# Kernel optimization log

Measured on AMD Instinct MI355X. Metric: run time of the kernel, lower is better.

## Reference

```python
import jax, jax.numpy as jnp
import numpy as np

S_DIM = 128            # attention head width s
E_DIM = 1024           # expansion e = 2*hidden
SQRT_S = 128.0 ** 0.5
EPS = 1e-5


def setup_inputs() -> dict:
    key = jax.random.key(0)
    ks = jax.random.split(key, 8)
    B, S, H = 64, 512, 512
    uv_dim = 2 * E_DIM + S_DIM  # 2176
    # xavier-uniform-ish scale for uv weight
    lim = (6.0 / (H + uv_dim)) ** 0.5
    return {
        "x": jax.random.normal(ks[0], (B, S, H), dtype=jnp.float32),
        "ln_g": jnp.ones((1,), dtype=jnp.float32),
        "uv_w": jax.random.uniform(ks[1], (uv_dim, H), minval=-lim, maxval=lim, dtype=jnp.float32),
        "uv_b": jnp.zeros((uv_dim,), dtype=jnp.float32),
        "gamma": jax.random.uniform(ks[2], (2, S_DIM), dtype=jnp.float32),
        "beta": jax.random.uniform(ks[3], (2, S_DIM), dtype=jnp.float32),
        "w_bias": jax.random.uniform(ks[4], (2 * S - 1,), dtype=jnp.float32),
        "o_w": jax.random.normal(ks[5], (H, E_DIM), dtype=jnp.float32) * 0.02,
        "o_b": jnp.zeros((H,), dtype=jnp.float32),
    }


def _rope(x):
    # x: [B, S, 2, s]; rotate along the sequence dim (dim=1)
    S = x.shape[1]
    half = x.shape[-1] // 2
    pos = jnp.arange(S, dtype=jnp.float32)
    # torch: freq_seq = -arange(half)/half; inv_freq = 10000**(-freq_seq)
    inv_freq = 10000.0 ** (jnp.arange(half, dtype=jnp.float32) / half)
    sinus = pos[:, None, None] * inv_freq[None, None, :]  # [S, 1, half]
    sin, cos = jnp.sin(sinus), jnp.cos(sinus)
    x1, x2 = x[..., :half], x[..., half:]
    return jnp.concatenate([x1 * cos - x2 * sin, x2 * cos + x1 * sin], axis=-1)


def reference(x, ln_g, uv_w, uv_b, gamma, beta, w_bias, o_w, o_b):
    B, S, H = x.shape
    # ScaleNorm
    norm = jnp.linalg.norm(x, axis=-1, keepdims=True) * (H ** -0.5)
    xn = x / jnp.maximum(norm, EPS) * ln_g
    # fused uv projection + SiLU
    act = jax.nn.silu(xn @ uv_w.T + uv_b)  # [B, S, 2e+s]
    u = act[..., :E_DIM]
    v = act[..., E_DIM:2 * E_DIM]
    base = act[..., 2 * E_DIM:]                      # [B, S, s]
    base = base[:, :, None, :] * gamma + beta        # [B, S, 2, s]
    base = _rope(base)
    q, k = base[:, :, 0, :], base[:, :, 1, :]
    # scores + relative position bias: bias[i, j] = w[j - i + S - 1]
    qk = jnp.einsum('bsd,btd->bst', q, k)
    idx = jnp.arange(S)[None, :] - jnp.arange(S)[:, None] + (S - 1)
    qk = qk + w_bias[idx]
    # relu2 similarity kernel
    kernel = jnp.square(jax.nn.relu(qk / SQRT_S))    # [B, S, S]
    out = u * jnp.einsum('bst,bte->bse', kernel, v)  # gated attention
    out = out @ o_w.T + o_b
    return out + x  # use_shortcut: hidden == output
```

## Files before the change

kernel.cpp:

```cpp
#include <hip/hip_runtime.h>
#include <math.h>


#define M_TOT   32768
#define S_LEN   512
#define H_DIM   512
#define E_DIMC  1024
#define UV_DIM  2176
#define UV_PAD  2304
#define D_DIM   128

using floatx4  = __attribute__((ext_vector_type(4))) float;
using uintx2   = __attribute__((ext_vector_type(2))) unsigned int;
using uintx4   = __attribute__((ext_vector_type(4))) unsigned int;
using ushortx4 = __attribute__((ext_vector_type(4))) unsigned short;
using short8   = __attribute__((ext_vector_type(8))) short;

#define ASYNC_CP16(gsrc, ldst)                                                  \
    __builtin_amdgcn_global_load_lds(                                           \
        (const __attribute__((address_space(1))) void*)(gsrc),                  \
        (__attribute__((address_space(3))) void*)(ldst), 16, 0, 0)

__device__ __forceinline__ float bf2f(unsigned short h) {
    union { unsigned int u; float f; } c;
    c.u = ((unsigned int)h) << 16;
    return c.f;
}
__device__ __forceinline__ unsigned short f2bf(float f) {
    union { float f; unsigned int u; } c;
    c.f = f;
    unsigned int r = c.u + 0x7fffu + ((c.u >> 16) & 1u);
    return (unsigned short)(r >> 16);
}
__device__ __forceinline__ float silu_fast(float x) {
    float e = __expf(-x);
    return x * __builtin_amdgcn_rcpf(1.0f + e);
}

__global__ __launch_bounds__(256) void f2bf_kernel(const float* __restrict__ in,
                                                   unsigned short* __restrict__ out,
                                                   int n4) {
    int i = blockIdx.x * 256 + threadIdx.x;
    if (i < n4) {
        floatx4 v = ((const floatx4*)in)[i];
        ushortx4 o;
        o.x = f2bf(v.x); o.y = f2bf(v.y); o.z = f2bf(v.z); o.w = f2bf(v.w);
        ((ushortx4*)out)[i] = o;
    }
}

__global__ __launch_bounds__(256) void f2bf_pad_kernel(const float* __restrict__ in,
                                                       unsigned short* __restrict__ out,
                                                       int n4_src, int n4_dst) {
    int i = blockIdx.x * 256 + threadIdx.x;
    if (i < n4_dst) {
        ushortx4 o;
        if (i < n4_src) {
            floatx4 v = ((const floatx4*)in)[i];
            o.x = f2bf(v.x); o.y = f2bf(v.y); o.z = f2bf(v.z); o.w = f2bf(v.w);
        } else {
            o.x = 0; o.y = 0; o.z = 0; o.w = 0;
        }
        ((ushortx4*)out)[i] = o;
    }
}

__global__ __launch_bounds__(256) void rmsnorm_kernel(const float* __restrict__ x,
                                                      const float* __restrict__ ln_g,
                                                      unsigned short* __restrict__ xn) {
    int row  = blockIdx.x * 4 + (threadIdx.x >> 6);
    int lane = threadIdx.x & 63;
    const float* xr = x + (size_t)row * H_DIM;
    floatx4 v0 = ((const floatx4*)xr)[lane];
    floatx4 v1 = ((const floatx4*)xr)[lane + 64];
    float ss = v0.x*v0.x + v0.y*v0.y + v0.z*v0.z + v0.w*v0.w
             + v1.x*v1.x + v1.y*v1.y + v1.z*v1.z + v1.w*v1.w;
    #pragma unroll
    for (int off = 32; off > 0; off >>= 1) ss += __shfl_xor(ss, off, 64);
    float norm = sqrtf(ss) * 0.044194173824159216f;
    float sc   = ln_g[0] / fmaxf(norm, 1e-5f);
    unsigned short* xo = xn + (size_t)row * H_DIM;
    ushortx4 o0, o1;
    o0.x = f2bf(v0.x * sc); o0.y = f2bf(v0.y * sc);
    o0.z = f2bf(v0.z * sc); o0.w = f2bf(v0.w * sc);
    o1.x = f2bf(v1.x * sc); o1.y = f2bf(v1.y * sc);
    o1.z = f2bf(v1.z * sc); o1.w = f2bf(v1.w * sc);
    ((ushortx4*)xo)[lane]      = o0;
    ((ushortx4*)xo)[lane + 64] = o1;
}

__global__ __launch_bounds__(64) void rope_table_kernel(float* __restrict__ cost,
                                                        float* __restrict__ sint) {
    int s = blockIdx.x;
    int j = threadIdx.x;
    float invf = (float)pow(10000.0, (double)j / 64.0);
    float ang  = (float)s * invf;
    double a   = (double)ang;
    cost[s * 64 + j] = (float)cos(a);
    sint[s * 64 + j] = (float)sin(a);
}

__global__ __launch_bounds__(256) void rope_apply_kernel(const float* __restrict__ base,
                                                         const float* __restrict__ gamma,
                                                         const float* __restrict__ beta,
                                                         const float* __restrict__ cost,
                                                         const float* __restrict__ sint,
                                                         unsigned short* __restrict__ q,
                                                         unsigned short* __restrict__ k) {
    int idx = blockIdx.x * 256 + threadIdx.x;
    int m = idx >> 6;
    int j = idx & 63;
    int s = m & (S_LEN - 1);
    float b1 = base[(size_t)m * D_DIM + j];
    float b2 = base[(size_t)m * D_DIM + 64 + j];
    float c  = cost[s * 64 + j];
    float sn = sint[s * 64 + j];
    float yq1 = b1 * gamma[j]       + beta[j];
    float yq2 = b2 * gamma[64 + j]  + beta[64 + j];
    float yk1 = b1 * gamma[128 + j] + beta[128 + j];
    float yk2 = b2 * gamma[192 + j] + beta[192 + j];
    q[(size_t)m * D_DIM + j]      = f2bf(yq1 * c - yq2 * sn);
    q[(size_t)m * D_DIM + 64 + j] = f2bf(yq2 * c + yq1 * sn);
    k[(size_t)m * D_DIM + j]      = f2bf(yk1 * c - yk2 * sn);
    k[(size_t)m * D_DIM + 64 + j] = f2bf(yk2 * c + yk1 * sn);
}

template <bool SWAPT>
__device__ __forceinline__ void gemm256_core(const unsigned short* __restrict__ A,
                                             const unsigned short* __restrict__ B,
                                             int lda, int ldb, int K,
                                             int m0, int n0,
                                             unsigned short (&st)[4][2][128][64],
                                             floatx4 (&acc)[8][4]) {
    const int tid  = threadIdx.x;
    const int lane = tid & 63;
    const int wave = tid >> 6;
    const int quad = lane >> 4;
    const int l16  = lane & 15;
    const int wrow = (wave >> 2) * 128;
    const int wcol = (wave & 3) * 64;

    const int q0    = wave * 128 + lane;
    const int R0    = q0 >> 3;
    const int cp0   = q0 & 7;
    const int c0    = cp0 ^ (R0 & 7);
    const int srow0 = 2 * R0 + (c0 >> 2);
    const int scol0 = (c0 & 3) * 8;

    const unsigned short* pa0 = A + (size_t)(m0 + srow0) * lda + scol0;
    const unsigned short* pa1 = pa0 + (size_t)16 * lda;
    const unsigned short* pb0 = B + (size_t)(n0 + srow0) * ldb + scol0;
    const unsigned short* pb1 = pb0 + (size_t)16 * ldb;
    const int ldsOff0 = (wave * 128) * 8;
    const int ldsOff1 = (wave * 128 + 64) * 8;

    #pragma unroll
    for (int i = 0; i < 8; i++)
        #pragma unroll
        for (int j = 0; j < 4; j++) acc[i][j] = (floatx4){0.f, 0.f, 0.f, 0.f};

    const int NT = K >> 5;
    auto stage = [&](int t) {
        unsigned short* sA = &st[t & 3][0][0][0];
        unsigned short* sB = &st[t & 3][1][0][0];
        const int kt = t * 32;
        ASYNC_CP16(pa0 + kt, sA + ldsOff0);
        ASYNC_CP16(pa1 + kt, sA + ldsOff1);
        ASYNC_CP16(pb0 + kt, sB + ldsOff0);
        ASYNC_CP16(pb1 + kt, sB + ldsOff1);
    };
    stage(0);
    stage(1);

    int aoff[8], boff[4];
    #pragma unroll
    for (int mt = 0; mt < 8; mt++) {
        int r  = wrow + mt * 16 + l16;
        int Rr = r >> 1;
        int cp = (((r & 1) << 2) + quad) ^ (Rr & 7);
        aoff[mt] = Rr * 64 + cp * 8;
    }
    #pragma unroll
    for (int nt = 0; nt < 4; nt++) {
        int r  = wcol + nt * 16 + l16;
        int Rr = r >> 1;
        int cp = (((r & 1) << 2) + quad) ^ (Rr & 7);
        boff[nt] = Rr * 64 + cp * 8;
    }

    for (int t = 0; t < NT; ++t) {
        if (t < NT - 1) asm volatile("s_waitcnt vmcnt(4)" ::: "memory");
        else            asm volatile("s_waitcnt vmcnt(0)" ::: "memory");
        __builtin_amdgcn_sched_barrier(0);
        __builtin_amdgcn_s_barrier();
        __builtin_amdgcn_sched_barrier(0);
        if (t + 2 < NT) stage(t + 2);

        const unsigned short* sA = &st[t & 3][0][0][0];
        const unsigned short* sB = &st[t & 3][1][0][0];
        short8 bf[4];
        #pragma unroll
        for (int nt = 0; nt < 4; nt++) {
            union { short8 s8; uintx4 u4; } fu;
            fu.u4 = *(const uintx4*)&sB[boff[nt]];
            bf[nt] = fu.s8;
        }
        #pragma unroll
        for (int half = 0; half < 2; half++) {
            short8 af[4];
            #pragma unroll
            for (int mt = 0; mt < 4; mt++) {
                union { short8 s8; uintx4 u4; } fu;
                fu.u4 = *(const uintx4*)&sA[aoff[half * 4 + mt]];
                af[mt] = fu.s8;
            }
            __builtin_amdgcn_s_setprio(1);
            #pragma unroll
            for (int mt = 0; mt < 4; mt++)
                #pragma unroll
                for (int nt = 0; nt < 4; nt++)
                    acc[half * 4 + mt][nt] = SWAPT
                        ? __builtin_amdgcn_mfma_f32_16x16x32_bf16(bf[nt], af[mt], acc[half * 4 + mt][nt], 0, 0, 0)
                        : __builtin_amdgcn_mfma_f32_16x16x32_bf16(af[mt], bf[nt], acc[half * 4 + mt][nt], 0, 0, 0);
            __builtin_amdgcn_s_setprio(0);
        }
    }
}

union __align__(16) Lds256 {
    unsigned short st[4][2][128][64];
    unsigned short T[256 * 256];
};

__global__ __launch_bounds__(512, 2) void gemm1_256_kernel(const unsigned short* __restrict__ xn,
                                                           const unsigned short* __restrict__ uvw,
                                                           const float* __restrict__ uvb,
                                                           unsigned short* __restrict__ u,
                                                           unsigned short* __restrict__ vT,
                                                           float* __restrict__ base) {
    __shared__ Lds256 lds;
    floatx4 acc[8][4];
    const int m0 = blockIdx.y * 256;
    const int xb = blockIdx.x;
    const int tid = threadIdx.x, lane = tid & 63, wave = tid >> 6;
    const int quad = lane >> 4, l16 = lane & 15;
    const int wrow = (wave >> 2) * 128, wcol = (wave & 3) * 64;

    if (xb < 4) {
        const int n0 = xb * 256;
        gemm256_core<true>(xn, uvw, H_DIM, H_DIM, H_DIM, m0, n0, lds.st, acc);
        __syncthreads();
        #pragma unroll
        for (int mt = 0; mt < 8; mt++) {
            int row = wrow + mt * 16 + l16;
            #pragma unroll
            for (int nt = 0; nt < 4; nt++) {
                int nl = wcol + nt * 16 + quad * 4;
                floatx4 b4 = *(const floatx4*)&uvb[n0 + nl];
                ushortx4 pk;
                #pragma unroll
                for (int r = 0; r < 4; r++)
                    pk[r] = f2bf(silu_fast(acc[mt][nt][r] + b4[r]));
                *(uintx2*)&lds.T[row * 256 + (((nl >> 3) ^ (row & 15)) & 31) * 8 + (nl & 7)] = *(uintx2*)&pk;
            }
        }
        __syncthreads();
        #pragma unroll
        for (int i = 0; i < 16; i++) {
            int idx = tid + i * 512;
            int row = idx >> 5, c16 = idx & 31;
            *(uintx4*)(u + (size_t)(m0 + row) * E_DIMC + n0 + c16 * 8) =
                *(const uintx4*)&lds.T[row * 256 + ((c16 ^ (row & 15)) * 8)];
        }
    } else if (xb < 8) {
        const int n0 = xb * 256;
        gemm256_core<false>(xn, uvw, H_DIM, H_DIM, H_DIM, m0, n0, lds.st, acc);
        __syncthreads();
        #pragma unroll
        for (int nt = 0; nt < 4; nt++) {
            int rowT = wcol + nt * 16 + l16;
            float bias = uvb[n0 + rowT];
            #pragma unroll
            for (int mt = 0; mt < 8; mt++) {
                int colT = wrow + mt * 16 + quad * 4;
                ushortx4 pk;
                #pragma unroll
                for (int r = 0; r < 4; r++)
                    pk[r] = f2bf(silu_fast(acc[mt][nt][r] + bias));
                *(uintx2*)&lds.T[rowT * 256 + (((colT >> 3) ^ (rowT & 15)) & 31) * 8 + (colT & 7)] = *(uintx2*)&pk;
            }
        }
        __syncthreads();
        const int b = m0 >> 9, sg0 = m0 & (S_LEN - 1), eg0 = n0 - E_DIMC;
        #pragma unroll
        for (int i = 0; i < 16; i++) {
            int idx = tid + i * 512;
            int e = idx >> 5, c16 = idx & 31;
            *(uintx4*)(vT + ((size_t)b * E_DIMC + eg0 + e) * S_LEN + sg0 + c16 * 8) =
                *(const uintx4*)&lds.T[e * 256 + ((c16 ^ (e & 15)) * 8)];
        }
    } else {
        const int n0 = 2048;
        gemm256_core<false>(xn, uvw, H_DIM, H_DIM, H_DIM, m0, n0, lds.st, acc);
        if ((wave & 3) < 2) {
            #pragma unroll
            for (int mt = 0; mt < 8; mt++) {
                int m = m0 + wrow + mt * 16 + quad * 4;
                #pragma unroll
                for (int nt = 0; nt < 4; nt++) {
                    int n = wcol + nt * 16 + l16;
                    float bias = uvb[2048 + n];
                    #pragma unroll
                    for (int r = 0; r < 4; r++)
                        base[(size_t)(m + r) * D_DIM + n] = silu_fast(acc[mt][nt][r] + bias);
                }
            }
        }
    }
}

__global__ __launch_bounds__(512, 2) void gemm_out256_kernel(const unsigned short* __restrict__ oe,
                                                             const unsigned short* __restrict__ ow,
                                                             const float* __restrict__ ob,
                                                             const float* __restrict__ x,
                                                             float* __restrict__ out) {
    __shared__ __align__(16) unsigned short st[4][2][128][64];
    floatx4 acc[8][4];
    const int m0 = blockIdx.y * 256, n0 = blockIdx.x * 256;
    gemm256_core<true>(oe, ow, E_DIMC, E_DIMC, E_DIMC, m0, n0, st, acc);

    const int tid = threadIdx.x, lane = tid & 63, wave = tid >> 6;
    const int quad = lane >> 4, l16 = lane & 15;
    const int wrow = (wave >> 2) * 128, wcol = (wave & 3) * 64;
    #pragma unroll
    for (int mt = 0; mt < 8; mt++) {
        int m = m0 + wrow + mt * 16 + l16;
        #pragma unroll
        for (int nt = 0; nt < 4; nt++) {
            int n = n0 + wcol + nt * 16 + quad * 4;
            size_t off = (size_t)m * H_DIM + n;
            floatx4 b4 = *(const floatx4*)&ob[n];
            floatx4 x4 = *(const floatx4*)&x[off];
            *(floatx4*)&out[off] = acc[mt][nt] + b4 + x4;
        }
    }
}

struct GemmLds {
    unsigned short As[128 * 64];
    unsigned short Bs[128 * 64];
};

template <bool SWAPT>
__device__ __forceinline__ void gemm_bt_core(const unsigned short* __restrict__ A,
                                             const unsigned short* __restrict__ B,
                                             int lda, int ldb, int K,
                                             int m0, int n0,
                                             GemmLds& lds, floatx4 (&acc)[4][4]) {
    const int tid  = threadIdx.x;
    const int lane = tid & 63;
    const int wave = tid >> 6;
    const int quad = lane >> 4;
    const int l16  = lane & 15;
    const int wm   = (wave >> 1) * 64;
    const int wn   = (wave & 1) * 64;
    const int lrow = lane >> 3;
    const int cgs  = ((lane & 7) ^ lrow) * 8;

    #pragma unroll
    for (int i = 0; i < 4; i++)
        #pragma unroll
        for (int j = 0; j < 4; j++) acc[i][j] = (floatx4){0.f, 0.f, 0.f, 0.f};

    for (int kt = 0; kt < K; kt += 64) {
        #pragma unroll
        for (int i = 0; i < 4; i++) {
            int r0 = wave * 32 + i * 8;
            const unsigned short* ga = A + (size_t)(m0 + r0 + lrow) * lda + kt + cgs;
            const unsigned short* gb = B + (size_t)(n0 + r0 + lrow) * ldb + kt + cgs;
            ASYNC_CP16(ga, &lds.As[r0 * 64]);
            ASYNC_CP16(gb, &lds.Bs[r0 * 64]);
        }
        __syncthreads();
        #pragma unroll
        for (int kk = 0; kk < 64; kk += 32) {
            short8 af[4], bf[4];
            const int pc = (kk + quad * 8) ^ ((l16 & 7) * 8);
            #pragma unroll
            for (int mt = 0; mt < 4; mt++) {
                int row = wm + mt * 16 + l16;
                union { short8 s8; uintx4 u4; } fu;
                fu.u4 = *(const uintx4*)&lds.As[row * 64 + pc];
                af[mt] = fu.s8;
            }
            #pragma unroll
            for (int nt = 0; nt < 4; nt++) {
                int row = wn + nt * 16 + l16;
                union { short8 s8; uintx4 u4; } fu;
                fu.u4 = *(const uintx4*)&lds.Bs[row * 64 + pc];
                bf[nt] = fu.s8;
            }
            #pragma unroll
            for (int mt = 0; mt < 4; mt++)
                #pragma unroll
                for (int nt = 0; nt < 4; nt++)
                    acc[mt][nt] = SWAPT
                        ? __builtin_amdgcn_mfma_f32_16x16x32_bf16(bf[nt], af[mt], acc[mt][nt], 0, 0, 0)
                        : __builtin_amdgcn_mfma_f32_16x16x32_bf16(af[mt], bf[nt], acc[mt][nt], 0, 0, 0);
        }
        __syncthreads();
    }
}

union LdsU {
    GemmLds g;
    unsigned short T[128 * 128];
};
__device__ __forceinline__ int swz(int row, int col) {
    return row * 128 + ((((col >> 3) ^ (row & 7)) << 3) | (col & 7));
}

__global__ __launch_bounds__(256) void gemm_qk_kernel(const unsigned short* __restrict__ q,
                                                      const unsigned short* __restrict__ k,
                                                      const float* __restrict__ wbias,
                                                      unsigned short* __restrict__ P) {
    __shared__ LdsU lds;
    floatx4 acc[4][4];
    size_t boff = (size_t)blockIdx.z * S_LEN * D_DIM;
    unsigned short* Pb = P + (size_t)blockIdx.z * S_LEN * S_LEN;
    const int m0 = blockIdx.x * 128, n0 = blockIdx.y * 128;
    gemm_bt_core<true>(q + boff, k + boff, D_DIM, D_DIM, D_DIM, m0, n0, lds.g, acc);

    const int tid = threadIdx.x, lane = tid & 63, wave = tid >> 6;
    const int quad = lane >> 4, l16 = lane & 15;
    const int wm = (wave >> 1) * 64, wn = (wave & 1) * 64;
    #pragma unroll
    for (int mt = 0; mt < 4; mt++) {
        int row = wm + mt * 16 + l16;
        int s   = m0 + row;
        #pragma unroll
        for (int nt = 0; nt < 4; nt++) {
            int nl = wn + nt * 16 + quad * 4;
            int t0 = n0 + nl;
            ushortx4 pk;
            #pragma unroll
            for (int r = 0; r < 4; r++) {
                float z = (acc[mt][nt][r] + wbias[t0 + r - s + (S_LEN - 1)]) * 0.08838834764831845f;
                z = fmaxf(z, 0.f);
                pk[r] = f2bf(z * z);
            }
            *(uintx2*)&lds.T[swz(row, nl)] = *(uintx2*)&pk;
        }
    }
    __syncthreads();
    #pragma unroll
    for (int i = 0; i < 8; i++) {
        int idx = tid + i * 256;
        int row = idx >> 4;
        int j   = idx & 15;
        *(uintx4*)(Pb + (size_t)(m0 + row) * S_LEN + n0 + j * 8) =
            *(const uintx4*)&lds.T[swz(row, j * 8)];
    }
}

__global__ __launch_bounds__(256) void gemm_pv_kernel(const unsigned short* __restrict__ P,
                                                      const unsigned short* __restrict__ vT,
                                                      unsigned short* __restrict__ u) {
    __shared__ LdsU lds;
    floatx4 acc[4][4];
    int bb = blockIdx.z;
    const unsigned short* Pb  = P  + (size_t)bb * S_LEN * S_LEN;
    const unsigned short* vTb = vT + (size_t)bb * E_DIMC * S_LEN;
    const int m0 = blockIdx.x * 128, n0 = blockIdx.y * 128;
    gemm_bt_core<true>(Pb, vTb, S_LEN, S_LEN, S_LEN, m0, n0, lds.g, acc);

    const int tid = threadIdx.x, lane = tid & 63, wave = tid >> 6;
    const int quad = lane >> 4, l16 = lane & 15;
    const int wm = (wave >> 1) * 64, wn = (wave & 1) * 64;
    #pragma unroll
    for (int mt = 0; mt < 4; mt++) {
        int row = wm + mt * 16 + l16;
        #pragma unroll
        for (int nt = 0; nt < 4; nt++) {
            int nl = wn + nt * 16 + quad * 4;
            ushortx4 pk;
            #pragma unroll
            for (int r = 0; r < 4; r++) pk[r] = f2bf(acc[mt][nt][r]);
            *(uintx2*)&lds.T[swz(row, nl)] = *(uintx2*)&pk;
        }
    }
    __syncthreads();
    #pragma unroll
    for (int i = 0; i < 8; i++) {
        int idx = tid + i * 256;
        int row = idx >> 4;
        int j   = idx & 15;
        size_t off = ((size_t)bb * S_LEN + m0 + row) * E_DIMC + n0 + j * 8;
        union { uintx4 u4; unsigned short s[8]; } tv, uv, ov;
        tv.u4 = *(const uintx4*)&lds.T[swz(row, j * 8)];
        uv.u4 = *(const uintx4*)(u + off);
        #pragma unroll
        for (int jj = 0; jj < 8; jj++) ov.s[jj] = f2bf(bf2f(tv.s[jj]) * bf2f(uv.s[jj]));
        *(uintx4*)(u + off) = ov.u4;
    }
}

extern "C" void kernel_launch(void* const* d_in, const int* in_sizes, int n_in,
                              void* d_out, int out_size, void* d_ws, size_t ws_size,
                              hipStream_t stream) {
    const float* x     = (const float*)d_in[0];
    const float* ln_g  = (const float*)d_in[1];
    const float* uv_w  = (const float*)d_in[2];
    const float* uv_b  = (const float*)d_in[3];
    const float* gamma = (const float*)d_in[4];
    const float* beta  = (const float*)d_in[5];
    const float* wbias = (const float*)d_in[6];
    const float* o_w   = (const float*)d_in[7];
    const float* o_b   = (const float*)d_in[8];
    float* out = (float*)d_out;

    char* ws = (char*)d_ws;
    size_t off = 0;
    auto alloc = [&](size_t bytes) {
        void* p = ws + off;
        off += (bytes + 255) & ~(size_t)255;
        return p;
    };
    unsigned short* u     = (unsigned short*)alloc((size_t)M_TOT * E_DIMC * 2);
    unsigned short* vT    = (unsigned short*)alloc((size_t)64 * E_DIMC * S_LEN * 2);
    unsigned short* xn    = (unsigned short*)alloc((size_t)M_TOT * H_DIM * 2);
    unsigned short* P     = xn;
    float*          base  = (float*)alloc((size_t)M_TOT * D_DIM * 4);
    unsigned short* q     = (unsigned short*)alloc((size_t)M_TOT * D_DIM * 2);
    unsigned short* k     = (unsigned short*)alloc((size_t)M_TOT * D_DIM * 2);
    float*          cost  = (float*)alloc((size_t)S_LEN * 64 * 4);
    float*          sint  = (float*)alloc((size_t)S_LEN * 64 * 4);
    unsigned short* uvwb  = (unsigned short*)alloc((size_t)UV_PAD * H_DIM * 2);
    unsigned short* owb   = (unsigned short*)alloc((size_t)H_DIM * E_DIMC * 2);
    (void)ws_size; (void)in_sizes; (void)n_in; (void)out_size;

    f2bf_pad_kernel<<<(UV_PAD * H_DIM / 4 + 255) / 256, 256, 0, stream>>>(
        uv_w, uvwb, UV_DIM * H_DIM / 4, UV_PAD * H_DIM / 4);
    f2bf_kernel<<<(H_DIM * E_DIMC / 4 + 255) / 256, 256, 0, stream>>>(o_w, owb, H_DIM * E_DIMC / 4);
    rope_table_kernel<<<S_LEN, 64, 0, stream>>>(cost, sint);

    rmsnorm_kernel<<<M_TOT / 4, 256, 0, stream>>>(x, ln_g, xn);

    gemm1_256_kernel<<<dim3(9, M_TOT / 256), 512, 0, stream>>>(xn, uvwb, uv_b, u, vT, base);

    rope_apply_kernel<<<M_TOT * 64 / 256, 256, 0, stream>>>(base, gamma, beta, cost, sint, q, k);

    gemm_qk_kernel<<<dim3(S_LEN / 128, S_LEN / 128, 64), 256, 0, stream>>>(q, k, wbias, P);

    gemm_pv_kernel<<<dim3(S_LEN / 128, E_DIMC / 128, 64), 256, 0, stream>>>(P, vT, u);

    gemm_out256_kernel<<<dim3(H_DIM / 256, M_TOT / 256), 512, 0, stream>>>(u, owb, o_b, x, out);
}
```

Before: 393.7 us.

## Remap workgroups across XCDs for L2 locality and deepen 256-tile prefetch

Adds an XCD-aware block index remap to the uv, output, QK and PV GEMM kernels. Consecutive logical tiles that share operands now land on the same XCD, so they can reuse that XCD's L2. It also deepens the 256-tile GEMM pipeline from two to three stages in flight, adjusting the vmcnt waits to match. The risk is that with four LDS buffers and three in flight, the stage written at t+3 reuses buffer (t-1)&3, which may still be read by lagging waves. The remap also assumes the grid sizes divide evenly by 8.

```diff
diff --git a/kernel.cpp b/kernel.cpp
--- a/kernel.cpp
+++ b/kernel.cpp
@@ -35,6 +35,9 @@
 __device__ __forceinline__ float silu_fast(float x) {
     float e = __expf(-x);
     return x * __builtin_amdgcn_rcpf(1.0f + e);
+}
+__device__ __forceinline__ int xcd_remap(int b, int nwg) {
+    return (b & 7) * (nwg >> 3) + (b >> 3);
 }
 
 __global__ __launch_bounds__(256) void f2bf_kernel(const float* __restrict__ in,
@@ -171,6 +174,7 @@
     };
     stage(0);
     stage(1);
+    stage(2);
 
     int aoff[8], boff[4];
     #pragma unroll
@@ -189,12 +193,13 @@
     }
 
     for (int t = 0; t < NT; ++t) {
-        if (t < NT - 1) asm volatile("s_waitcnt vmcnt(4)" ::: "memory");
-        else            asm volatile("s_waitcnt vmcnt(0)" ::: "memory");
+        if (t < NT - 2)       asm volatile("s_waitcnt vmcnt(8)" ::: "memory");
+        else if (t == NT - 2) asm volatile("s_waitcnt vmcnt(4)" ::: "memory");
+        else                  asm volatile("s_waitcnt vmcnt(0)" ::: "memory");
         __builtin_amdgcn_sched_barrier(0);
         __builtin_amdgcn_s_barrier();
         __builtin_amdgcn_sched_barrier(0);
-        if (t + 2 < NT) stage(t + 2);
+        if (t + 3 < NT) stage(t + 3);
 
         const unsigned short* sA = &st[t & 3][0][0][0];
         const unsigned short* sB = &st[t & 3][1][0][0];
@@ -240,8 +245,10 @@
                                                            float* __restrict__ base) {
     __shared__ Lds256 lds;
     floatx4 acc[8][4];
-    const int m0 = blockIdx.y * 256;
-    const int xb = blockIdx.x;
+    const int bl = blockIdx.y * 9 + blockIdx.x;
+    const int lg = xcd_remap(bl, 9 * (M_TOT / 256));
+    const int xb = lg % 9;
+    const int m0 = (lg / 9) * 256;
     const int tid = threadIdx.x, lane = tid & 63, wave = tid >> 6;
     const int quad = lane >> 4, l16 = lane & 15;
     const int wrow = (wave >> 2) * 128, wcol = (wave & 3) * 64;
@@ -326,7 +333,10 @@
                                                              float* __restrict__ out) {
     __shared__ __align__(16) unsigned short st[4][2][128][64];
     floatx4 acc[8][4];
-    const int m0 = blockIdx.y * 256, n0 = blockIdx.x * 256;
+    const int bl = blockIdx.y * 2 + blockIdx.x;
+    const int lg = xcd_remap(bl, 2 * (M_TOT / 256));
+    const int n0 = (lg & 1) * 256;
+    const int m0 = (lg >> 1) * 256;
     gemm256_core<true>(oe, ow, E_DIMC, E_DIMC, E_DIMC, m0, n0, st, acc);
 
     const int tid = threadIdx.x, lane = tid & 63, wave = tid >> 6;
@@ -426,9 +436,12 @@
                                                       unsigned short* __restrict__ P) {
     __shared__ LdsU lds;
     floatx4 acc[4][4];
-    size_t boff = (size_t)blockIdx.z * S_LEN * D_DIM;
-    unsigned short* Pb = P + (size_t)blockIdx.z * S_LEN * S_LEN;
-    const int m0 = blockIdx.x * 128, n0 = blockIdx.y * 128;
+    const int bl = (blockIdx.z * 4 + blockIdx.y) * 4 + blockIdx.x;
+    const int lg = xcd_remap(bl, 1024);
+    const int bx = lg & 3, by = (lg >> 2) & 3, bz = lg >> 4;
+    size_t boff = (size_t)bz * S_LEN * D_DIM;
+    unsigned short* Pb = P + (size_t)bz * S_LEN * S_LEN;
+    const int m0 = bx * 128, n0 = by * 128;
     gemm_bt_core<true>(q + boff, k + boff, D_DIM, D_DIM, D_DIM, m0, n0, lds.g, acc);
 
     const int tid = threadIdx.x, lane = tid & 63, wave = tid >> 6;
@@ -468,10 +481,12 @@
                                                       unsigned short* __restrict__ u) {
     __shared__ LdsU lds;
     floatx4 acc[4][4];
-    int bb = blockIdx.z;
+    const int bl = (blockIdx.z * 8 + blockIdx.y) * 4 + blockIdx.x;
+    const int lg = xcd_remap(bl, 2048);
+    const int bx = lg & 3, by = (lg >> 2) & 7, bb = lg >> 5;
     const unsigned short* Pb  = P  + (size_t)bb * S_LEN * S_LEN;
     const unsigned short* vTb = vT + (size_t)bb * E_DIMC * S_LEN;
-    const int m0 = blockIdx.x * 128, n0 = blockIdx.y * 128;
+    const int m0 = bx * 128, n0 = by * 128;
     gemm_bt_core<true>(Pb, vTb, S_LEN, S_LEN, S_LEN, m0, n0, lds.g, acc);
 
     const int tid = threadIdx.x, lane = tid & 63, wave = tid >> 6;
```

After: 368.7 us. 1.07x faster.
